# Kernel tuning notes

Hardware: AMD Instinct MI355X
Metric: run time of the kernel (lower is better)

## Reference

```python
import jax, jax.numpy as jnp
import numpy as np
import math

E, K, CAPF = 8, 2, 1.25
D, DFF = 512, 2048


def setup_inputs() -> dict:
    key = jax.random.key(0)
    ks = jax.random.split(key, 5)
    s = lambda k, sh, sc: (jax.random.normal(k, sh, jnp.float32) * sc)
    return {
        "x": jax.random.normal(ks[0], (8, 4096, D), jnp.float32),
        "Wr": s(ks[1], (D, E), 1.0 / math.sqrt(D)),
        "br": jnp.zeros((E,), jnp.float32),
        "W1": s(ks[2], (E, D, DFF), 1.0 / math.sqrt(D)),
        "b1": jnp.zeros((E, DFF), jnp.float32),
        "W2": s(ks[3], (E, DFF, D), 1.0 / math.sqrt(DFF)),
        "b2": jnp.zeros((E, D), jnp.float32),
    }


def _moe(x, Wr, br, W1, b1, W2, b2):
    orig = x.shape
    d = orig[-1]
    xf = x.reshape(-1, d)                     # [N, d]
    N = xf.shape[0]
    # --- TopK router ---
    logits = xf @ Wr + br                      # [N, E]
    probs = jax.nn.softmax(logits, axis=-1)
    topk_p, topk_i = jax.lax.top_k(probs, K)   # [N, K]
    topk_w = topk_p / (jnp.sum(topk_p, axis=-1, keepdims=True) + 1e-9)
    # --- Capacity-based sparse dispatch ---
    cap = max(1, int(math.ceil(CAPF * float(N * K) / float(E))))
    flat_e = topk_i.reshape(-1)                # [N*K] expert id per slot
    flat_w = topk_w.reshape(-1)                # [N*K]
    tok = jnp.repeat(jnp.arange(N), K)         # [N*K] source token id
    one_hot = jax.nn.one_hot(flat_e, E, dtype=xf.dtype)          # [N*K, E]
    pos = (jnp.cumsum(one_hot, axis=0) - one_hot)[jnp.arange(N * K), flat_e]
    pos = pos.astype(jnp.int32)                # position within expert buffer
    keep = pos < cap                           # tokens beyond capacity dropped
    w_k = jnp.where(keep, flat_w, 0.0)
    sum_w = jnp.zeros((N,), xf.dtype).at[tok].add(w_k)           # kept weight per token
    w_norm = w_k / (sum_w[tok] + 1e-9)
    slot = flat_e * cap + pos                  # flat index into [E*cap]
    slot_safe = jnp.where(keep, slot, E * cap) # out-of-bounds -> dropped by scatter
    expert_in = (jnp.zeros((E * cap, d), xf.dtype)
                 .at[slot_safe].set(xf[tok], mode="drop")
                 .reshape(E, cap, d))
    # --- Grouped expert FFN (exact GELU like torch nn.GELU) ---
    h = jax.nn.gelu(jnp.einsum("ecd,edf->ecf", expert_in, W1) + b1[:, None, :],
                    approximate=False)
    expert_out = (jnp.einsum("ecf,efd->ecd", h, W2) + b2[:, None, :]).reshape(E * cap, d)
    # --- Combine: gather back and weighted scatter-add per token ---
    contrib = expert_out[jnp.where(keep, slot, 0)]               # dropped -> w_norm=0
    y = jnp.zeros((N, d), xf.dtype).at[tok].add(contrib * w_norm[:, None])
    return y.reshape(orig)


def reference(x, Wr, br, W1, b1, W2, b2):
    return _moe(x, Wr, br, W1, b1, W2, b2)
```

## Files before the change

### kernel.cpp

```cpp
#include <hip/hip_runtime.h>
#include <cstdint>
#include <cstddef>

#define E_EXP 8
#define TOPK 2
#define DMODEL 512
#define DFFDIM 2048

typedef __attribute__((ext_vector_type(8))) short short8;
typedef __attribute__((ext_vector_type(4))) float f32x4;

__device__ __forceinline__ unsigned short f2bf(float f) {
    unsigned int u = __float_as_uint(f);
    u += 0x7fffu + ((u >> 16) & 1u);
    return (unsigned short)(u >> 16);
}

__global__ __launch_bounds__(256) void transpose_kernel(
    const float* __restrict__ in, unsigned short* __restrict__ out, int R, int C)
{
    __shared__ float tile[32][33];
    const float* ie = in + (size_t)blockIdx.z * R * C;
    unsigned short* oe = out + (size_t)blockIdx.z * R * C;
    int x = blockIdx.x * 32 + threadIdx.x;
#pragma unroll
    for (int i = 0; i < 4; i++) {
        int ry = blockIdx.y * 32 + threadIdx.y + i * 8;
        tile[threadIdx.y + i * 8][threadIdx.x] = ie[(size_t)ry * C + x];
    }
    __syncthreads();
    int xo = blockIdx.y * 32 + threadIdx.x;
#pragma unroll
    for (int i = 0; i < 4; i++) {
        int co = blockIdx.x * 32 + threadIdx.y + i * 8;
        oe[(size_t)co * R + xo] = f2bf(tile[threadIdx.x][threadIdx.y + i * 8]);
    }
}

__global__ __launch_bounds__(256) void router_kernel(
    const float* __restrict__ x, const float* __restrict__ Wr,
    const float* __restrict__ br, int N,
    int* __restrict__ e0e1, float2* __restrict__ w01)
{
    int lane = threadIdx.x & 63, wave = threadIdx.x >> 6;
    int t = blockIdx.x * 4 + wave;
    if (t >= N) return;
    const float* xr = x + (size_t)t * DMODEL;
    float4 v0 = *(const float4*)(xr + lane * 4);
    float4 v1 = *(const float4*)(xr + 256 + lane * 4);
    float xv[8] = {v0.x, v0.y, v0.z, v0.w, v1.x, v1.y, v1.z, v1.w};
    const float* wr0 = Wr + (size_t)lane * 32;
    const float* wr1 = Wr + (size_t)(256 + lane * 4) * 8;
    double acc[8];
#pragma unroll
    for (int j = 0; j < 8; j++) acc[j] = 0.0;
#pragma unroll
    for (int c = 0; c < 4; c++) {
#pragma unroll
        for (int j = 0; j < 8; j++) {
            acc[j] += (double)xv[c] * (double)wr0[c * 8 + j];
            acc[j] += (double)xv[4 + c] * (double)wr1[c * 8 + j];
        }
    }
#pragma unroll
    for (int j = 0; j < 8; j++) {
        double s = acc[j];
#pragma unroll
        for (int o = 32; o > 0; o >>= 1) s += __shfl_xor(s, o, 64);
        acc[j] = s;
    }
    if (lane == 0) {
        float l[8], p[8];
        float mx = -1e30f;
        for (int j = 0; j < 8; j++) { l[j] = (float)acc[j] + br[j]; mx = fmaxf(mx, l[j]); }
        float Z = 0.f;
        for (int j = 0; j < 8; j++) { p[j] = expf(l[j] - mx); Z += p[j]; }
        for (int j = 0; j < 8; j++) p[j] /= Z;
        int e0 = 0;
        for (int j = 1; j < 8; j++) if (l[j] > l[e0]) e0 = j;
        int e1 = (e0 == 0) ? 1 : 0;
        for (int j = 0; j < 8; j++) if (j != e0 && l[j] > l[e1]) e1 = j;
        float den = p[e0] + p[e1] + 1e-9f;
        e0e1[t] = e0 | (e1 << 8);
        w01[t] = make_float2(p[e0] / den, p[e1] / den);
    }
}

__global__ __launch_bounds__(256) void hist_kernel(
    const int* __restrict__ e0e1, int NK, int* __restrict__ hist)
{
    __shared__ int cnt[8];
    int t = threadIdx.x;
    if (t < 8) cnt[t] = 0;
    __syncthreads();
    int s = blockIdx.x * 256 + t;
    if (s < NK) {
        int pk = e0e1[s >> 1];
        int e = (s & 1) ? ((pk >> 8) & 255) : (pk & 255);
        atomicAdd(&cnt[e], 1);
    }
    __syncthreads();
    if (t < 8) hist[blockIdx.x * 8 + t] = cnt[t];
}

__global__ __launch_bounds__(256) void scan_kernel(
    const int* __restrict__ hist, int NB, int cap,
    int* __restrict__ base, int* __restrict__ cnt_used)
{
    __shared__ int buf[256];
    int t = threadIdx.x;
    for (int e = 0; e < 8; e++) {
        int v = (t < NB) ? hist[t * 8 + e] : 0;
        int val = v;
        buf[t] = val;
        __syncthreads();
        for (int o = 1; o < 256; o <<= 1) {
            int add = (t >= o) ? buf[t - o] : 0;
            __syncthreads();
            val += add;
            buf[t] = val;
            __syncthreads();
        }
        if (t < NB) base[t * 8 + e] = val - v;
        if (t == 255) cnt_used[e] = min(val, cap);
        __syncthreads();
    }
}

__global__ __launch_bounds__(256) void pos_kernel(
    const int* __restrict__ e0e1, const float2* __restrict__ w01,
    const int* __restrict__ base, int NK, int cap,
    int* __restrict__ sidx, int* __restrict__ tok_of, float* __restrict__ wslot)
{
    __shared__ int waveCnt[4][8];
    __shared__ float kw[256];
    int t = threadIdx.x, lane = t & 63, wave = t >> 6;
    int s = blockIdx.x * 256 + t;
    bool valid = s < NK;
    int e = 8; float w = 0.f;
    if (valid) {
        int pk = e0e1[s >> 1];
        float2 ww = w01[s >> 1];
        if (s & 1) { e = (pk >> 8) & 255; w = ww.y; }
        else       { e = pk & 255;        w = ww.x; }
    }
    unsigned long long mymask = 0ull;
#pragma unroll
    for (int j = 0; j < 8; j++) {
        unsigned long long m = __ballot(e == j);
        if (lane == j) waveCnt[wave][j] = __popcll(m);
        if (e == j) mymask = m;
    }
    __syncthreads();
    int wrank = __popcll(mymask & ((1ull << lane) - 1ull));
    int prior = 0;
    for (int w2 = 0; w2 < wave; w2++) prior += waveCnt[w2][e & 7];
    int pos = base[blockIdx.x * 8 + (e & 7)] + prior + wrank;
    bool keep = valid && (pos < cap);
    kw[t] = keep ? w : 0.f;
    __syncthreads();
    float sum = kw[t] + kw[t ^ 1];
    float wn = keep ? (kw[t] / (sum + 1e-9f)) : 0.f;
    if (valid) {
        int si = keep ? (e * cap + pos) : -1;
        sidx[s] = si;
        if (keep) { tok_of[si] = s >> 1; wslot[si] = wn; }
    }
}

__global__ __launch_bounds__(256) void scatter_kernel(
    const float* __restrict__ x, const int* __restrict__ sidx,
    unsigned short* __restrict__ Xe, int NK)
{
    int lane = threadIdx.x & 63, wave = threadIdx.x >> 6;
    int s = blockIdx.x * 4 + wave;
    if (s >= NK) return;
    int si = sidx[s];
    if (si < 0) return;
    int tok = s >> 1;
    const float* xr = x + (size_t)tok * DMODEL + lane * 8;
    float4 a = *(const float4*)xr;
    float4 b = *(const float4*)(xr + 4);
    short8 v;
    v[0] = (short)f2bf(a.x); v[1] = (short)f2bf(a.y);
    v[2] = (short)f2bf(a.z); v[3] = (short)f2bf(a.w);
    v[4] = (short)f2bf(b.x); v[5] = (short)f2bf(b.y);
    v[6] = (short)f2bf(b.z); v[7] = (short)f2bf(b.w);
    *(short8*)(Xe + (size_t)si * DMODEL + lane * 8) = v;
}

template <int MODE>
__global__ __launch_bounds__(256, 3) void gemm_kernel(
    const unsigned short* __restrict__ A, int lda, size_t aStrE,
    const unsigned short* __restrict__ B, int ldb, size_t bStrE,
    const float* __restrict__ bias, int biasStrE,
    void* __restrict__ out, size_t cStrE, int ldc,
    const int* __restrict__ cnt, const int* __restrict__ tok_of,
    const float* __restrict__ wslot, int cap, int Kext)
{
    __shared__ unsigned short As[2][128 * 32];
    __shared__ unsigned short Bs[2][128 * 32];
    int e = blockIdx.z;
    int m0 = blockIdx.y * 128, n0 = blockIdx.x * 128;
    int M = cnt[e];
    if (m0 >= M) return;
    const unsigned short* Ae = A + (size_t)e * aStrE;
    const unsigned short* Be = B + (size_t)e * bStrE;

    int t = threadIdx.x, lane = t & 63, wave = t >> 6;
    int row = t >> 2, seg = (t & 3) * 8;
    const unsigned short* ga = Ae + (size_t)(m0 + row) * lda + seg;
    const unsigned short* gb = Be + (size_t)(n0 + row) * ldb + seg;
    unsigned short* la0 = &As[0][t * 8];
    unsigned short* la1 = &As[0][(t + 256) * 8];
    unsigned short* lb0 = &Bs[0][t * 8];
    unsigned short* lb1 = &Bs[0][(t + 256) * 8];

    f32x4 acc[4][4];
#pragma unroll
    for (int i = 0; i < 4; i++)
#pragma unroll
        for (int j = 0; j < 4; j++) acc[i][j] = (f32x4){0.f, 0.f, 0.f, 0.f};

    int wm = (wave & 1) * 64, wn = (wave >> 1) * 64;
    int lr = lane & 15, lq = lane >> 4;
    const unsigned short* pa = &As[0][(wm + lr) * 32 + lq * 8];
    const unsigned short* pb = &Bs[0][(wn + lr) * 32 + lq * 8];

    short8 ra0 = *(const short8*)ga;
    short8 ra1 = *(const short8*)(ga + (size_t)64 * lda);
    short8 rb0 = *(const short8*)gb;
    short8 rb1 = *(const short8*)(gb + (size_t)64 * ldb);
    ga += 32; gb += 32;
    *(short8*)la0 = ra0; *(short8*)la1 = ra1;
    *(short8*)lb0 = rb0; *(short8*)lb1 = rb1;
    __syncthreads();

    int buf = 0;
    for (int k0 = 32; k0 < Kext; k0 += 32) {
        ra0 = *(const short8*)ga;
        ra1 = *(const short8*)(ga + (size_t)64 * lda);
        rb0 = *(const short8*)gb;
        rb1 = *(const short8*)(gb + (size_t)64 * ldb);
        ga += 32; gb += 32;
        {
            int bo = buf * (128 * 32);
            short8 af[4], bf[4];
#pragma unroll
            for (int i = 0; i < 4; i++) af[i] = *(const short8*)(pa + bo + i * 16 * 32);
#pragma unroll
            for (int j = 0; j < 4; j++) bf[j] = *(const short8*)(pb + bo + j * 16 * 32);
#pragma unroll
            for (int i = 0; i < 4; i++)
#pragma unroll
                for (int j = 0; j < 4; j++)
                    acc[i][j] = __builtin_amdgcn_mfma_f32_16x16x32_bf16(af[i], bf[j], acc[i][j], 0, 0, 0);
        }
        int nbo = (buf ^ 1) * (128 * 32);
        *(short8*)(la0 + nbo) = ra0; *(short8*)(la1 + nbo) = ra1;
        *(short8*)(lb0 + nbo) = rb0; *(short8*)(lb1 + nbo) = rb1;
        __syncthreads();
        buf ^= 1;
    }
    {
        int bo = buf * (128 * 32);
        short8 af[4], bf[4];
#pragma unroll
        for (int i = 0; i < 4; i++) af[i] = *(const short8*)(pa + bo + i * 16 * 32);
#pragma unroll
        for (int j = 0; j < 4; j++) bf[j] = *(const short8*)(pb + bo + j * 16 * 32);
#pragma unroll
        for (int i = 0; i < 4; i++)
#pragma unroll
            for (int j = 0; j < 4; j++)
                acc[i][j] = __builtin_amdgcn_mfma_f32_16x16x32_bf16(af[i], bf[j], acc[i][j], 0, 0, 0);
    }

    if (MODE == 0) {
        size_t cb = (size_t)e * cStrE;
#pragma unroll
        for (int j = 0; j < 4; j++) {
            int n = n0 + wn + j * 16 + lr;
            float bv = bias[(size_t)e * biasStrE + n];
#pragma unroll
            for (int i = 0; i < 4; i++) {
                int mbase = m0 + wm + i * 16 + lq * 4;
                f32x4 v = acc[i][j];
#pragma unroll
                for (int r = 0; r < 4; r++) {
                    float val = v[r] + bv;
                    val = 0.5f * val * (1.0f + erff(val * 0.7071067811865475f));
                    ((unsigned short*)out)[cb + (size_t)(mbase + r) * ldc + n] = f2bf(val);
                }
            }
        }
    } else {
        float wv[4][4]; int tv[4][4];
#pragma unroll
        for (int i = 0; i < 4; i++) {
            int mbase = m0 + wm + i * 16 + lq * 4;
#pragma unroll
            for (int r = 0; r < 4; r++) {
                int m = mbase + r;
                if (m < M) { int sl = e * cap + m; wv[i][r] = wslot[sl]; tv[i][r] = tok_of[sl]; }
                else       { wv[i][r] = 0.f; tv[i][r] = -1; }
            }
        }
        float* y = (float*)out;
#pragma unroll
        for (int j = 0; j < 4; j++) {
            int n = n0 + wn + j * 16 + lr;
            float bv = bias[(size_t)e * biasStrE + n];
#pragma unroll
            for (int i = 0; i < 4; i++) {
                f32x4 v = acc[i][j];
#pragma unroll
                for (int r = 0; r < 4; r++) {
                    if (tv[i][r] >= 0)
                        atomicAdd(y + (size_t)tv[i][r] * ldc + n, wv[i][r] * (v[r] + bv));
                }
            }
        }
    }
}

extern "C" void kernel_launch(void* const* d_in, const int* in_sizes, int n_in,
                              void* d_out, int out_size, void* d_ws, size_t ws_size,
                              hipStream_t stream)
{
    const float* x  = (const float*)d_in[0];
    const float* Wr = (const float*)d_in[1];
    const float* br = (const float*)d_in[2];
    const float* W1 = (const float*)d_in[3];
    const float* b1 = (const float*)d_in[4];
    const float* W2 = (const float*)d_in[5];
    const float* b2 = (const float*)d_in[6];
    float* y = (float*)d_out;
    (void)n_in;

    const int N = in_sizes[0] / DMODEL;
    const int NK = N * TOPK;
    const int cap = (NK * 5 + 31) / 32;
    const int mTiles = (cap + 127) / 128;
    const int NB = (NK + 255) / 256;

    size_t fixed = (size_t)E_EXP * DMODEL * DFFDIM * 2 * 2
                 + (size_t)E_EXP * cap * DMODEL * 2
                 + (size_t)N * 12 + (size_t)NK * 4 + (size_t)E_EXP * cap * 8
                 + (size_t)NB * 64 + (1 << 16);
    int G = E_EXP;
    while (G > 1 && fixed + (size_t)G * cap * DFFDIM * 2 > ws_size) G >>= 1;
    const int nGroups = E_EXP / G;

    char* ws = (char*)d_ws;
    size_t off = 0;
    auto take = [&](size_t bytes) {
        char* p = ws + off;
        off = (off + bytes + 255) & ~(size_t)255;
        return p;
    };
    unsigned short* W1t = (unsigned short*)take((size_t)E_EXP * DMODEL * DFFDIM * 2);
    unsigned short* W2t = (unsigned short*)take((size_t)E_EXP * DMODEL * DFFDIM * 2);
    unsigned short* Xe  = (unsigned short*)take((size_t)E_EXP * cap * DMODEL * 2);
    unsigned short* Hg  = (unsigned short*)take((size_t)G * cap * DFFDIM * 2);
    int*    e0e1 = (int*)take((size_t)N * 4);
    float2* w01  = (float2*)take((size_t)N * 8);
    int*    hist = (int*)take((size_t)NB * 8 * 4);
    int*    base = (int*)take((size_t)NB * 8 * 4);
    int*    cnt  = (int*)take(64);
    int*    sidx = (int*)take((size_t)NK * 4);
    int*    tok_of = (int*)take((size_t)E_EXP * cap * 4);
    float*  wslot  = (float*)take((size_t)E_EXP * cap * 4);

    transpose_kernel<<<dim3(DFFDIM / 32, DMODEL / 32, E_EXP), dim3(32, 8), 0, stream>>>(W1, W1t, DMODEL, DFFDIM);
    transpose_kernel<<<dim3(DMODEL / 32, DFFDIM / 32, E_EXP), dim3(32, 8), 0, stream>>>(W2, W2t, DFFDIM, DMODEL);
    router_kernel<<<(N + 3) / 4, 256, 0, stream>>>(x, Wr, br, N, e0e1, w01);
    hist_kernel<<<NB, 256, 0, stream>>>(e0e1, NK, hist);
    scan_kernel<<<1, 256, 0, stream>>>(hist, NB, cap, base, cnt);
    pos_kernel<<<NB, 256, 0, stream>>>(e0e1, w01, base, NK, cap, sidx, tok_of, wslot);
    scatter_kernel<<<(NK + 3) / 4, 256, 0, stream>>>(x, sidx, Xe, NK);
    hipMemsetAsync(d_out, 0, (size_t)out_size * 4, stream);

    for (int g = 0; g < nGroups; g++) {
        int e0 = g * G;
        gemm_kernel<0><<<dim3(DFFDIM / 128, mTiles, G), 256, 0, stream>>>(
            Xe + (size_t)e0 * cap * DMODEL, DMODEL, (size_t)cap * DMODEL,
            W1t + (size_t)e0 * DFFDIM * DMODEL, DMODEL, (size_t)DFFDIM * DMODEL,
            b1 + (size_t)e0 * DFFDIM, DFFDIM,
            Hg, (size_t)cap * DFFDIM, DFFDIM,
            cnt + e0, tok_of, wslot, cap, DMODEL);
        gemm_kernel<1><<<dim3(DMODEL / 128, mTiles, G), 256, 0, stream>>>(
            Hg, DFFDIM, (size_t)cap * DFFDIM,
            W2t + (size_t)e0 * DMODEL * DFFDIM, DFFDIM, (size_t)DMODEL * DFFDIM,
            b2 + (size_t)e0 * DMODEL, DMODEL,
            y, 0, DMODEL,
            cnt + e0, tok_of + (size_t)e0 * cap, wslot + (size_t)e0 * cap, cap, DFFDIM);
    }
}
```

Measured before the change: 998.2 us.

## Load GEMM tiles directly global-to-LDS with XOR-swizzled layout

Replaces the register-staged global loads and LDS stores in the grouped expert GEMM with global_load_lds direct-to-LDS transfers. It also XOR-swizzles the 8-element segments within each tile row to reduce LDS bank conflicts on fragment reads. The goal is to free VGPRs and the VALU store instructions while keeping the copy for the next stage overlapped with MFMA. The change relies on the global_load_lds wave-contiguous placement matching the swizzled read indexing, and on __syncthreads being enough to order those asynchronous loads.

```diff
diff --git a/kernel.cpp b/kernel.cpp
--- a/kernel.cpp
+++ b/kernel.cpp
@@ -14,6 +14,12 @@
     unsigned int u = __float_as_uint(f);
     u += 0x7fffu + ((u >> 16) & 1u);
     return (unsigned short)(u >> 16);
+}
+
+__device__ __forceinline__ void gld_lds16(const unsigned short* g, unsigned short* l) {
+    __builtin_amdgcn_global_load_lds(
+        (const __attribute__((address_space(1))) void*)g,
+        (__attribute__((address_space(3))) void*)l, 16, 0, 0);
 }
 
 __global__ __launch_bounds__(256) void transpose_kernel(
@@ -198,8 +204,8 @@
     const int* __restrict__ cnt, const int* __restrict__ tok_of,
     const float* __restrict__ wslot, int cap, int Kext)
 {
-    __shared__ unsigned short As[2][128 * 32];
-    __shared__ unsigned short Bs[2][128 * 32];
+    __shared__ unsigned short As[2 * 128 * 32];
+    __shared__ unsigned short Bs[2 * 128 * 32];
     int e = blockIdx.z;
     int m0 = blockIdx.y * 128, n0 = blockIdx.x * 128;
     int M = cnt[e];
@@ -208,13 +214,11 @@
     const unsigned short* Be = B + (size_t)e * bStrE;
 
     int t = threadIdx.x, lane = t & 63, wave = t >> 6;
-    int row = t >> 2, seg = (t & 3) * 8;
+    int row = t >> 2;
+    int seg = ((t & 3) ^ ((t >> 3) & 3)) * 8;
     const unsigned short* ga = Ae + (size_t)(m0 + row) * lda + seg;
     const unsigned short* gb = Be + (size_t)(n0 + row) * ldb + seg;
-    unsigned short* la0 = &As[0][t * 8];
-    unsigned short* la1 = &As[0][(t + 256) * 8];
-    unsigned short* lb0 = &Bs[0][t * 8];
-    unsigned short* lb1 = &Bs[0][(t + 256) * 8];
+    int wofs = __builtin_amdgcn_readfirstlane(wave * 512);
 
     f32x4 acc[4][4];
 #pragma unroll
@@ -224,56 +228,53 @@
 
     int wm = (wave & 1) * 64, wn = (wave >> 1) * 64;
     int lr = lane & 15, lq = lane >> 4;
-    const unsigned short* pa = &As[0][(wm + lr) * 32 + lq * 8];
-    const unsigned short* pb = &Bs[0][(wn + lr) * 32 + lq * 8];
-
-    short8 ra0 = *(const short8*)ga;
-    short8 ra1 = *(const short8*)(ga + (size_t)64 * lda);
-    short8 rb0 = *(const short8*)gb;
-    short8 rb1 = *(const short8*)(gb + (size_t)64 * ldb);
+    int sq = (lq ^ ((lr >> 1) & 3)) * 8;
+    const unsigned short* pa = As + (wm + lr) * 32 + sq;
+    const unsigned short* pb = Bs + (wn + lr) * 32 + sq;
+
+    gld_lds16(ga, As + wofs);
+    gld_lds16(ga + (size_t)64 * lda, As + 2048 + wofs);
+    gld_lds16(gb, Bs + wofs);
+    gld_lds16(gb + (size_t)64 * ldb, Bs + 2048 + wofs);
     ga += 32; gb += 32;
-    *(short8*)la0 = ra0; *(short8*)la1 = ra1;
-    *(short8*)lb0 = rb0; *(short8*)lb1 = rb1;
     __syncthreads();
 
     int buf = 0;
     for (int k0 = 32; k0 < Kext; k0 += 32) {
-        ra0 = *(const short8*)ga;
-        ra1 = *(const short8*)(ga + (size_t)64 * lda);
-        rb0 = *(const short8*)gb;
-        rb1 = *(const short8*)(gb + (size_t)64 * ldb);
+        int nbo = (buf ^ 1) * 4096;
+        gld_lds16(ga, As + nbo + wofs);
+        gld_lds16(ga + (size_t)64 * lda, As + nbo + 2048 + wofs);
+        gld_lds16(gb, Bs + nbo + wofs);
+        gld_lds16(gb + (size_t)64 * ldb, Bs + nbo + 2048 + wofs);
         ga += 32; gb += 32;
         {
-            int bo = buf * (128 * 32);
-            short8 af[4], bf[4];
-#pragma unroll
-            for (int i = 0; i < 4; i++) af[i] = *(const short8*)(pa + bo + i * 16 * 32);
-#pragma unroll
-            for (int j = 0; j < 4; j++) bf[j] = *(const short8*)(pb + bo + j * 16 * 32);
+            int bo = buf * 4096;
+            short8 af[4], bfv[4];
+#pragma unroll
+            for (int i = 0; i < 4; i++) af[i] = *(const short8*)(pa + bo + i * 512);
+#pragma unroll
+            for (int j = 0; j < 4; j++) bfv[j] = *(const short8*)(pb + bo + j * 512);
 #pragma unroll
             for (int i = 0; i < 4; i++)
 #pragma unroll
                 for (int j = 0; j < 4; j++)
-                    acc[i][j] = __builtin_amdgcn_mfma_f32_16x16x32_bf16(af[i], bf[j], acc[i][j], 0, 0, 0);
-        }
-        int nbo = (buf ^ 1) * (128 * 32);
-        *(short8*)(la0 + nbo) = ra0; *(short8*)(la1 + nbo) = ra1;
-        *(short8*)(lb0 + nbo) = rb0; *(short8*)(lb1 + nbo) = rb1;
+                    acc[i][j] = __builtin_amdgcn_mfma_f32_16x16x32_bf16(af[i], bfv[j], acc[i][j], 0, 0, 0);
+        }
         __syncthreads();
         buf ^= 1;
     }
     {
-        int bo = buf * (128 * 32);
-        short8 af[4], bf[4];
-#pragma unroll
-        for (int i = 0; i < 4; i++) af[i] = *(const short8*)(pa + bo + i * 16 * 32);
-#pragma unroll
-        for (int j = 0; j < 4; j++) bf[j] = *(const short8*)(pb + bo + j * 16 * 32);
+        int bo = buf * 4096;
+        short8 af[4], bfv[4];
+#pragma unroll
+        for (int i = 0; i < 4; i++) af[i] = *(const short8*)(pa + bo + i * 512);
+#pragma unroll
+        for (int j = 0; j < 4; j++) bfv[j] = *(const short8*)(pb + bo + j * 512);
 #pragma unroll
         for (int i = 0; i < 4; i++)
 #pragma unroll
             for (int j = 0; j < 4; j++)
-                acc[i][j] = __builtin_amdgcn_mfma_f32_16x16x32_bf16(af[i], bf[j], acc[i][j], 0, 0, 0);
+                acc[i][j] = __builtin_amdgcn_mfma_f32_16x16x32_bf16(af[i], bfv[j], acc[i][j], 0, 0, 0);
     }
 
     if (MODE == 0) {
```

After: 993.6 us. About the same (-0.5%).
